# Optimization experiments

Hardware: AMD Instinct MI355X
Metric: run time of the kernel (lower is better)

The kernel has to match this reference:

```python
import jax, jax.numpy as jnp
import numpy as np
import math

B, N, WIDTH, HEADS = 2, 2048, 1024, 16
ATTN_CH = WIDTH // HEADS  # 64 (note: width//heads//3 of the 3*width fused dim)


def setup_inputs() -> dict:
    key = jax.random.key(0)
    ks = jax.random.split(key, 3)
    std = 0.02
    return {
        "x": jax.random.normal(ks[0], (B, N, WIDTH), dtype=jnp.float32),
        "w_qkv": jax.random.normal(ks[1], (WIDTH, 3 * WIDTH), dtype=jnp.float32) * std,
        "b_qkv": jnp.zeros((3 * WIDTH,), dtype=jnp.float32),
        "w_proj": jax.random.normal(ks[2], (WIDTH, WIDTH), dtype=jnp.float32) * std,
        "b_proj": jnp.zeros((WIDTH,), dtype=jnp.float32),
    }


def reference(x, w_qkv, b_qkv, w_proj, b_proj):
    bs, n_ctx, width = x.shape
    qkv = x @ w_qkv + b_qkv                       # [b, n, 3*width]
    attn_ch = (3 * width) // HEADS // 3           # head dim
    scale = 1.0 / math.sqrt(math.sqrt(attn_ch))
    # per-head layout: [b, n, heads, 3*attn_ch] -> split q,k,v
    qkv = qkv.reshape(bs, n_ctx, HEADS, 3 * attn_ch)
    q, k, v = jnp.split(qkv, 3, axis=-1)          # each [b, n, h, c]
    weight = jnp.einsum("bthc,bshc->bhts", q * scale, k * scale)
    weight = jax.nn.softmax(weight.astype(jnp.float32), axis=-1).astype(qkv.dtype)
    out = jnp.einsum("bhts,bshc->bthc", weight, v).reshape(bs, n_ctx, -1)
    return out @ w_proj + b_proj
```

## Files before the change

### kernel.cpp

```cpp
#include <hip/hip_runtime.h>
#include <hip/hip_fp16.h>

#define BATCH 2
#define NCTX  2048
#define WIDTH 1024
#define HEADS 16
#define CH    64
#define QKVD  (3 * WIDTH)
#define MROWS (BATCH * NCTX)

typedef __attribute__((ext_vector_type(4))) float    f32x4;
typedef __attribute__((ext_vector_type(8))) _Float16 f16x8;

#define QSCALE 0.18033688011112042f

__device__ __forceinline__ void gll16(void* lds, const void* g) {
    __builtin_amdgcn_global_load_lds(
        (const __attribute__((address_space(1))) unsigned int*)g,
        (__attribute__((address_space(3))) unsigned int*)lds, 16, 0, 0);
}

__device__ __forceinline__ unsigned pkrtz(float a, float b) {
    auto p = __builtin_amdgcn_cvt_pkrtz(a, b);
    return __builtin_bit_cast(unsigned, p);
}

__global__ __launch_bounds__(256)
void split_x_f16(const float* __restrict__ x, __half* __restrict__ tiles)
{
    const int mb = blockIdx.x, kt = blockIdx.y;
    const int t = threadIdx.x;
    __half* tb = (__half*)tiles + ((size_t)mb * 32 + kt) * 4096;
    #pragma unroll
    for (int it = 0; it < 2; ++it) {
        const int idx = it * 256 + t;
        const int m = idx >> 2, q = idx & 3;
        const float* src = x + (size_t)(mb * 128 + m) * WIDTH + kt * 32 + q * 8;
        const f32x4 v0 = *(const f32x4*)src;
        const f32x4 v1 = *(const f32x4*)(src + 4);
        f16x8 h;
        #pragma unroll
        for (int j = 0; j < 4; ++j) { h[j] = (_Float16)v0[j]; h[4 + j] = (_Float16)v1[j]; }
        *(f16x8*)&tb[(q * 128 + m) * 8] = h;
    }
}

__global__ __launch_bounds__(256)
void split_w_f16(const float* __restrict__ w, __half* __restrict__ tiles, int N)
{
    __shared__ float tile[32][129];
    const int nb = blockIdx.x, kt = blockIdx.y;
    const int t = threadIdx.x;
    #pragma unroll
    for (int it = 0; it < 2; ++it) {
        const int idx = it * 256 + t;
        const int kk = idx >> 4, n8 = idx & 15;
        const float* src = w + (size_t)(kt * 32 + kk) * N + nb * 128 + n8 * 8;
        #pragma unroll
        for (int j = 0; j < 8; ++j) tile[kk][n8 * 8 + j] = src[j];
    }
    __syncthreads();
    __half* tb = tiles + ((size_t)nb * 32 + kt) * 4096;
    #pragma unroll
    for (int it = 0; it < 2; ++it) {
        const int idx = it * 256 + t;
        const int q = idx >> 7, nn = idx & 127;
        f16x8 h;
        #pragma unroll
        for (int j = 0; j < 8; ++j) h[j] = (_Float16)tile[q * 8 + j][nn];
        *(f16x8*)&tb[(q * 128 + nn) * 8] = h;
    }
}

__global__ __launch_bounds__(256)
void gemm_qkv(const __half* __restrict__ At, const __half* __restrict__ Bt,
              const float* __restrict__ bias,
              __half* __restrict__ qg, __half* __restrict__ kg, __half* __restrict__ vtg)
{
    __shared__ __align__(16) _Float16 sm[16384];
    const int t = threadIdx.x, lane = t & 63, w = t >> 6;
    const int lq = lane & 15, quad = lane >> 4;
    const int nb = blockIdx.x, mb = blockIdx.y;
    const int wm = (w >> 1) * 64, wn = (w & 1) * 64;

    const __half* Ab = At + ((size_t)mb * 32) * 4096;
    const __half* Bb = Bt + ((size_t)nb * 32) * 4096;
    const int c0 = w * 4;

    f32x4 acc[4][4];
    #pragma unroll
    for (int i = 0; i < 4; ++i)
        #pragma unroll
        for (int j = 0; j < 4; ++j) acc[i][j] = 0;

    f16x8 pf[4];
    #pragma unroll
    for (int i = 0; i < 4; ++i) {
        const int c = c0 + i;
        const __half* g = (c < 8 ? Ab + c * 512 : Bb + (c - 8) * 512) + lane * 8;
        pf[i] = *(const f16x8*)g;
    }
    #pragma unroll
    for (int i = 0; i < 4; ++i)
        *(f16x8*)&sm[(c0 + i) * 512 + lane * 8] = pf[i];
    __syncthreads();

    for (int kt = 0; kt < 32; ++kt) {
        _Float16* cur = sm + (kt & 1) * 8192;
        _Float16* nxt = sm + ((kt + 1) & 1) * 8192;

        if (kt + 1 < 32) {
            #pragma unroll
            for (int i = 0; i < 4; ++i) {
                const int c = c0 + i;
                const __half* g = (c < 8 ? Ab + (size_t)(kt + 1) * 4096 + c * 512
                                         : Bb + (size_t)(kt + 1) * 4096 + (c - 8) * 512) + lane * 8;
                pf[i] = *(const f16x8*)g;
            }
        }

        f16x8 a[4], b[4];
        #pragma unroll
        for (int i = 0; i < 4; ++i) {
            a[i] = *(const f16x8*)&cur[(quad * 128 + wm + i * 16 + lq) * 8];
            b[i] = *(const f16x8*)&cur[4096 + (quad * 128 + wn + i * 16 + lq) * 8];
        }
        #pragma unroll
        for (int i = 0; i < 4; ++i)
            #pragma unroll
            for (int j = 0; j < 4; ++j)
                acc[i][j] = __builtin_amdgcn_mfma_f32_16x16x32_f16(a[i], b[j], acc[i][j], 0, 0, 0);

        if (kt + 1 < 32) {
            #pragma unroll
            for (int i = 0; i < 4; ++i)
                *(f16x8*)&nxt[(c0 + i) * 512 + lane * 8] = pf[i];
        }
        __syncthreads();
    }

    const int bb = mb >> 4;
    #pragma unroll
    for (int jf = 0; jf < 4; ++jf) {
        const int col = nb * 128 + wn + jf * 16 + lq;
        const int h = col / 192;
        const int sect = col - h * 192;
        const int type = sect >> 6;
        const int c = sect & 63;
        const float bv = bias[col];
        const size_t bh = (size_t)bb * 16 + h;
        #pragma unroll
        for (int i = 0; i < 4; ++i) {
            #pragma unroll
            for (int r = 0; r < 4; ++r) {
                const int n = (mb & 15) * 128 + wm + i * 16 + quad * 4 + r;
                const float v = acc[i][jf][r] + bv;
                if (type == 0) {
                    const size_t a2 = ((bh * 16 + (n >> 7)) * 8 + (c >> 3)) * 1024
                                      + (size_t)(n & 127) * 8 + (c & 7);
                    qg[a2] = __float2half(v * QSCALE);
                } else if (type == 1) {
                    const size_t a2 = ((bh * 32 + (n >> 6)) * 8 + (c >> 3)) * 512
                                      + (size_t)(n & 63) * 8 + (c & 7);
                    kg[a2] = __float2half(v);
                } else {
                    const size_t a2 = ((bh * 32 + (n >> 6)) * 8 + ((n >> 3) & 7)) * 512
                                      + (size_t)c * 8 + (n & 7);
                    vtg[a2] = __float2half(v);
                }
            }
        }
    }
}

__global__ __launch_bounds__(256)
void attn_mfma3(const __half* __restrict__ qg, const __half* __restrict__ kg,
                const __half* __restrict__ vtg, __half* __restrict__ a2)
{
    __shared__ __align__(16) _Float16 Ks[2][4096];
    __shared__ __align__(16) _Float16 Vt[2][4096];
    __shared__ __align__(16) _Float16 Ps[16384];

    const int t = threadIdx.x, lane = t & 63, w = t >> 6;
    const int lq = lane & 15, quad = lane >> 4;
    const int bid = blockIdx.x;
    const int qt2 = (bid >> 3) & 15;
    const int bh_ = (bid & 7) + ((bid >> 7) << 3);
    const size_t bh = (size_t)bh_;
    const int h = bh_ & 15, b = bh_ >> 4;

    const __half* qtile = qg + (bh * 16 + qt2) * 8192;
    const __half* kbase = kg + bh * 32 * 4096;
    const __half* vbase = vtg + bh * 32 * 4096;

    #pragma unroll
    for (int i = 0; i < 4; ++i)
        gll16((void*)&Ps[(w * 4 + i) * 512], (const void*)(qtile + (w * 4 + i) * 512 + lane * 8));

    const int lw = w * 2 * 512 + lane * 8;
    f16x8 kpf[2], vpf[2], vheld[2];
    #pragma unroll
    for (int i = 0; i < 2; ++i) {
        kpf[i] = *(const f16x8*)(kbase + lw + i * 512);
        vpf[i] = *(const f16x8*)(vbase + lw + i * 512);
    }
    __syncthreads();

    #pragma unroll
    for (int i = 0; i < 2; ++i) {
        *(f16x8*)&Ks[0][lw + i * 512] = kpf[i];
        *(f16x8*)&Vt[0][lw + i * 512] = vpf[i];
    }
    f16x8 aq[2][2];
    #pragma unroll
    for (int qn = 0; qn < 2; ++qn)
        #pragma unroll
        for (int ks = 0; ks < 2; ++ks)
            aq[qn][ks] = *(const f16x8*)&Ps[((ks * 4 + quad) * 128 + w * 32 + qn * 16 + lq) * 8];
    __syncthreads();

    f32x4 O[2][4], Ol[2];
    #pragma unroll
    for (int qn = 0; qn < 2; ++qn) {
        Ol[qn] = 0;
        #pragma unroll
        for (int j = 0; j < 4; ++j) O[qn][j] = 0;
    }
    f16x8 ones;
    #pragma unroll
    for (int j = 0; j < 8; ++j) ones[j] = (_Float16)1.0f;

    _Float16* PwBase = &Ps[w * 4096];
    const int kb_hi = quad >> 1, joff = (quad & 1) * 4;
    const f32x4 zc = {0.0f, 0.0f, 0.0f, 0.0f};

    const __half* kp = kbase + 4096 + lw;
    const __half* vp = vbase + 4096 + lw;

    for (int kt = 0; kt < 32; ++kt) {
        const int cur = kt & 1;

        if (kt < 31) {
            kpf[0] = *(const f16x8*)(kp);
            kpf[1] = *(const f16x8*)(kp + 512);
            vpf[0] = *(const f16x8*)(vp);
            vpf[1] = *(const f16x8*)(vp + 512);
            kp += 4096; vp += 4096;
        }

        f32x4 st[4][2];
        #pragma unroll
        for (int mt = 0; mt < 4; ++mt) {
            f16x8 kf0 = *(const f16x8*)&Ks[cur][((quad) * 64 + mt * 16 + lq) * 8];
            f16x8 kf1 = *(const f16x8*)&Ks[cur][((4 + quad) * 64 + mt * 16 + lq) * 8];
            st[mt][0] = __builtin_amdgcn_mfma_f32_16x16x32_f16(kf0, aq[0][0], zc, 0, 0, 0);
            st[mt][1] = __builtin_amdgcn_mfma_f32_16x16x32_f16(kf0, aq[1][0], zc, 0, 0, 0);
            st[mt][0] = __builtin_amdgcn_mfma_f32_16x16x32_f16(kf1, aq[0][1], st[mt][0], 0, 0, 0);
            st[mt][1] = __builtin_amdgcn_mfma_f32_16x16x32_f16(kf1, aq[1][1], st[mt][1], 0, 0, 0);
        }

        if (kt > 0) {
            const int pv = (kt - 1) & 1;
            _Float16* Pr = PwBase + pv * 2048;
            #pragma unroll
            for (int ks = 0; ks < 2; ++ks) {
                f16x8 ap0 = *(const f16x8*)&Pr[((ks * 4 + quad) * 32 + lq) * 8];
                f16x8 ap1 = *(const f16x8*)&Pr[((ks * 4 + quad) * 32 + 16 + lq) * 8];
                Ol[0] = __builtin_amdgcn_mfma_f32_16x16x32_f16(ap0, ones, Ol[0], 0, 0, 0);
                Ol[1] = __builtin_amdgcn_mfma_f32_16x16x32_f16(ap1, ones, Ol[1], 0, 0, 0);
                #pragma unroll
                for (int jc = 0; jc < 4; ++jc) {
                    f16x8 vf = *(const f16x8*)&Vt[pv][((ks * 4 + quad) * 64 + jc * 16 + lq) * 8];
                    O[0][jc] = __builtin_amdgcn_mfma_f32_16x16x32_f16(ap0, vf, O[0][jc], 0, 0, 0);
                    O[1][jc] = __builtin_amdgcn_mfma_f32_16x16x32_f16(ap1, vf, O[1][jc], 0, 0, 0);
                }
            }
        }

        {
            _Float16* Pww = PwBase + cur * 2048;
            #pragma unroll
            for (int mt = 0; mt < 4; ++mt) {
                #pragma unroll
                for (int qn = 0; qn < 2; ++qn) {
                    const float e0 = __builtin_amdgcn_exp2f(st[mt][qn][0]);
                    const float e1 = __builtin_amdgcn_exp2f(st[mt][qn][1]);
                    const float e2 = __builtin_amdgcn_exp2f(st[mt][qn][2]);
                    const float e3 = __builtin_amdgcn_exp2f(st[mt][qn][3]);
                    uint2 pk;
                    pk.x = pkrtz(e0, e1);
                    pk.y = pkrtz(e2, e3);
                    *(uint2*)&Pww[((mt * 2 + kb_hi) * 32 + qn * 16 + lq) * 8 + joff] = pk;
                }
            }
        }

        if (kt < 31) {
            *(f16x8*)&Ks[cur ^ 1][lw] = kpf[0];
            *(f16x8*)&Ks[cur ^ 1][lw + 512] = kpf[1];
        }
        if (kt > 0) {
            *(f16x8*)&Vt[cur][lw] = vheld[0];
            *(f16x8*)&Vt[cur][lw + 512] = vheld[1];
        }
        vheld[0] = vpf[0]; vheld[1] = vpf[1];
        __syncthreads();
    }

    {
        _Float16* Pr = PwBase + 1 * 2048;
        #pragma unroll
        for (int ks = 0; ks < 2; ++ks) {
            f16x8 ap0 = *(const f16x8*)&Pr[((ks * 4 + quad) * 32 + lq) * 8];
            f16x8 ap1 = *(const f16x8*)&Pr[((ks * 4 + quad) * 32 + 16 + lq) * 8];
            Ol[0] = __builtin_amdgcn_mfma_f32_16x16x32_f16(ap0, ones, Ol[0], 0, 0, 0);
            Ol[1] = __builtin_amdgcn_mfma_f32_16x16x32_f16(ap1, ones, Ol[1], 0, 0, 0);
            #pragma unroll
            for (int jc = 0; jc < 4; ++jc) {
                f16x8 vf = *(const f16x8*)&Vt[1][((ks * 4 + quad) * 64 + jc * 16 + lq) * 8];
                O[0][jc] = __builtin_amdgcn_mfma_f32_16x16x32_f16(ap0, vf, O[0][jc], 0, 0, 0);
                O[1][jc] = __builtin_amdgcn_mfma_f32_16x16x32_f16(ap1, vf, O[1][jc], 0, 0, 0);
            }
        }
    }

    float linv[2][4];
    #pragma unroll
    for (int qn = 0; qn < 2; ++qn)
        #pragma unroll
        for (int r = 0; r < 4; ++r)
            linv[qn][r] = 1.0f / Ol[qn][r];

    __half* a2t = a2 + ((size_t)b * 16 + qt2) * 32 * 4096;
    #pragma unroll
    for (int jc = 0; jc < 4; ++jc) {
        const int ch = h * 64 + jc * 16 + lq;
        const int ktp = ch >> 5;
        const int qc = (ch >> 3) & 3;
        const int j = ch & 7;
        #pragma unroll
        for (int qn = 0; qn < 2; ++qn)
            #pragma unroll
            for (int r = 0; r < 4; ++r) {
                const int m = w * 32 + qn * 16 + quad * 4 + r;
                a2t[(size_t)ktp * 4096 + (qc * 128 + m) * 8 + j] =
                    __float2half(O[qn][jc][r] * linv[qn][r]);
            }
    }
}

__global__ __launch_bounds__(256)
void gemm_proj(const __half* __restrict__ At, const __half* __restrict__ Bt,
               const float* __restrict__ bias, float* __restrict__ out)
{
    __shared__ __align__(16) _Float16 sm[16384];
    const int t = threadIdx.x, lane = t & 63, w = t >> 6;
    const int lq = lane & 15, quad = lane >> 4;
    const int nb = blockIdx.x, mb = blockIdx.y;
    const int wm = (w >> 1) * 64, wn = (w & 1) * 64;

    const __half* Ab = At + ((size_t)mb * 32) * 4096;
    const __half* Bb = Bt + ((size_t)nb * 32) * 4096;
    const int c0 = w * 4;

    f32x4 acc[4][4];
    #pragma unroll
    for (int i = 0; i < 4; ++i)
        #pragma unroll
        for (int j = 0; j < 4; ++j) acc[i][j] = 0;

    f16x8 pf[4];
    #pragma unroll
    for (int i = 0; i < 4; ++i) {
        const int c = c0 + i;
        const __half* g = (c < 8 ? Ab + c * 512 : Bb + (c - 8) * 512) + lane * 8;
        pf[i] = *(const f16x8*)g;
    }
    #pragma unroll
    for (int i = 0; i < 4; ++i)
        *(f16x8*)&sm[(c0 + i) * 512 + lane * 8] = pf[i];
    __syncthreads();

    for (int kt = 0; kt < 32; ++kt) {
        _Float16* cur = sm + (kt & 1) * 8192;
        _Float16* nxt = sm + ((kt + 1) & 1) * 8192;

        if (kt + 1 < 32) {
            #pragma unroll
            for (int i = 0; i < 4; ++i) {
                const int c = c0 + i;
                const __half* g = (c < 8 ? Ab + (size_t)(kt + 1) * 4096 + c * 512
                                         : Bb + (size_t)(kt + 1) * 4096 + (c - 8) * 512) + lane * 8;
                pf[i] = *(const f16x8*)g;
            }
        }

        f16x8 a[4], b[4];
        #pragma unroll
        for (int i = 0; i < 4; ++i) {
            a[i] = *(const f16x8*)&cur[(quad * 128 + wm + i * 16 + lq) * 8];
            b[i] = *(const f16x8*)&cur[4096 + (quad * 128 + wn + i * 16 + lq) * 8];
        }
        #pragma unroll
        for (int i = 0; i < 4; ++i)
            #pragma unroll
            for (int j = 0; j < 4; ++j)
                acc[i][j] = __builtin_amdgcn_mfma_f32_16x16x32_f16(a[i], b[j], acc[i][j], 0, 0, 0);

        if (kt + 1 < 32) {
            #pragma unroll
            for (int i = 0; i < 4; ++i)
                *(f16x8*)&nxt[(c0 + i) * 512 + lane * 8] = pf[i];
        }
        __syncthreads();
    }

    #pragma unroll
    for (int jf = 0; jf < 4; ++jf) {
        const int col = nb * 128 + wn + jf * 16 + lq;
        const float bv = bias[col];
        #pragma unroll
        for (int i = 0; i < 4; ++i)
            #pragma unroll
            for (int r = 0; r < 4; ++r) {
                const int row = mb * 128 + wm + i * 16 + quad * 4 + r;
                out[(size_t)row * WIDTH + col] = acc[i][jf][r] + bv;
            }
    }
}

extern "C" void kernel_launch(void* const* d_in, const int* in_sizes, int n_in,
                              void* d_out, int out_size, void* d_ws, size_t ws_size,
                              hipStream_t stream)
{
    const float* x      = (const float*)d_in[0];
    const float* w_qkv  = (const float*)d_in[1];
    const float* b_qkv  = (const float*)d_in[2];
    const float* w_proj = (const float*)d_in[3];
    const float* b_proj = (const float*)d_in[4];
    float* out = (float*)d_out;

    char* p = (char*)d_ws;
    size_t o = 0;
    __half* A1  = (__half*)(p + o); o += (size_t)MROWS * WIDTH * 2;
    __half* Bq  = (__half*)(p + o); o += (size_t)WIDTH * QKVD * 2;
    __half* Qg  = (__half*)(p + o); o += (size_t)MROWS * WIDTH * 2;
    __half* Kg  = (__half*)(p + o); o += (size_t)MROWS * WIDTH * 2;
    __half* Vtg = (__half*)(p + o); o += (size_t)MROWS * WIDTH * 2;
    __half* A2  = (__half*)(p + o); o += (size_t)MROWS * WIDTH * 2;
    __half* Bp  = (__half*)(p + o); o += (size_t)WIDTH * WIDTH * 2;

    dim3 blk(256);

    split_x_f16<<<dim3(32, 32), blk, 0, stream>>>(x, A1);
    split_w_f16<<<dim3(24, 32), blk, 0, stream>>>(w_qkv, Bq, QKVD);
    split_w_f16<<<dim3(8, 32),  blk, 0, stream>>>(w_proj, Bp, WIDTH);

    gemm_qkv<<<dim3(24, 32), blk, 0, stream>>>(A1, Bq, b_qkv, Qg, Kg, Vtg);

    attn_mfma3<<<dim3(512), blk, 0, stream>>>(Qg, Kg, Vtg, A2);

    gemm_proj<<<dim3(8, 32), blk, 0, stream>>>(A2, Bp, b_proj, out);
}
```

Measured before the change: 197.5 us.

## Halve attention query tile per block and drop P double-buffer software pipeline

The attention kernel now processes 64 query rows per block (16 per wave) instead of 128, doubling the grid to 1024 blocks and shrinking the P scratch in LDS from 32KB to 8KB. The cross-iteration pipelining, where the PV product of the previous tile overlapped the QK of the current one, is removed. P is now computed and consumed within the same iteration, and V is stored straight into the next buffer. This aims to raise occupancy and parallelism through lower register and LDS use, at the cost of re-reading K/V twice as often and losing MFMA/exp overlap within a wave.

```diff
diff --git a/kernel.cpp b/kernel.cpp
--- a/kernel.cpp
+++ b/kernel.cpp
@@ -174,31 +174,32 @@
 }
 
 __global__ __launch_bounds__(256)
-void attn_mfma3(const __half* __restrict__ qg, const __half* __restrict__ kg,
+void attn_mfma5(const __half* __restrict__ qg, const __half* __restrict__ kg,
                 const __half* __restrict__ vtg, __half* __restrict__ a2)
 {
     __shared__ __align__(16) _Float16 Ks[2][4096];
     __shared__ __align__(16) _Float16 Vt[2][4096];
-    __shared__ __align__(16) _Float16 Ps[16384];
+    __shared__ __align__(16) _Float16 Ps[4096];
 
     const int t = threadIdx.x, lane = t & 63, w = t >> 6;
     const int lq = lane & 15, quad = lane >> 4;
     const int bid = blockIdx.x;
-    const int qt2 = (bid >> 3) & 15;
-    const int bh_ = (bid & 7) + ((bid >> 7) << 3);
+    const int qt = (bid >> 3) & 31;
+    const int bh_ = (bid & 7) + ((bid >> 8) << 3);
     const size_t bh = (size_t)bh_;
     const int h = bh_ & 15, b = bh_ >> 4;
 
-    const __half* qtile = qg + (bh * 16 + qt2) * 8192;
+    const __half* qtile = qg + (bh * 16 + (qt >> 1)) * 8192 + (size_t)(qt & 1) * 512;
     const __half* kbase = kg + bh * 32 * 4096;
     const __half* vbase = vtg + bh * 32 * 4096;
 
     #pragma unroll
-    for (int i = 0; i < 4; ++i)
-        gll16((void*)&Ps[(w * 4 + i) * 512], (const void*)(qtile + (w * 4 + i) * 512 + lane * 8));
-
-    const int lw = w * 2 * 512 + lane * 8;
-    f16x8 kpf[2], vpf[2], vheld[2];
+    for (int i = 0; i < 2; ++i)
+        gll16((void*)&Ps[(w * 2 + i) * 512],
+              (const void*)(qtile + (size_t)(w * 2 + i) * 1024 + lane * 8));
+
+    const int lw = w * 1024 + lane * 8;
+    f16x8 kpf[2], vpf[2];
     #pragma unroll
     for (int i = 0; i < 2; ++i) {
         kpf[i] = *(const f16x8*)(kbase + lw + i * 512);
@@ -211,26 +212,21 @@
         *(f16x8*)&Ks[0][lw + i * 512] = kpf[i];
         *(f16x8*)&Vt[0][lw + i * 512] = vpf[i];
     }
-    f16x8 aq[2][2];
-    #pragma unroll
-    for (int qn = 0; qn < 2; ++qn)
-        #pragma unroll
-        for (int ks = 0; ks < 2; ++ks)
-            aq[qn][ks] = *(const f16x8*)&Ps[((ks * 4 + quad) * 128 + w * 32 + qn * 16 + lq) * 8];
+    f16x8 aq[2];
+    #pragma unroll
+    for (int ks = 0; ks < 2; ++ks)
+        aq[ks] = *(const f16x8*)&Ps[((ks * 4 + quad) * 64 + w * 16 + lq) * 8];
     __syncthreads();
 
-    f32x4 O[2][4], Ol[2];
-    #pragma unroll
-    for (int qn = 0; qn < 2; ++qn) {
-        Ol[qn] = 0;
-        #pragma unroll
-        for (int j = 0; j < 4; ++j) O[qn][j] = 0;
-    }
+    f32x4 O[4], Ol;
+    Ol = 0;
+    #pragma unroll
+    for (int j = 0; j < 4; ++j) O[j] = 0;
     f16x8 ones;
     #pragma unroll
     for (int j = 0; j < 8; ++j) ones[j] = (_Float16)1.0f;
 
-    _Float16* PwBase = &Ps[w * 4096];
+    _Float16* Pw = &Ps[w * 1024];
     const int kb_hi = quad >> 1, joff = (quad & 1) * 4;
     const f32x4 zc = {0.0f, 0.0f, 0.0f, 0.0f};
 
@@ -248,90 +244,53 @@
             kp += 4096; vp += 4096;
         }
 
-        f32x4 st[4][2];
+        f32x4 st[4];
         #pragma unroll
         for (int mt = 0; mt < 4; ++mt) {
             f16x8 kf0 = *(const f16x8*)&Ks[cur][((quad) * 64 + mt * 16 + lq) * 8];
             f16x8 kf1 = *(const f16x8*)&Ks[cur][((4 + quad) * 64 + mt * 16 + lq) * 8];
-            st[mt][0] = __builtin_amdgcn_mfma_f32_16x16x32_f16(kf0, aq[0][0], zc, 0, 0, 0);
-            st[mt][1] = __builtin_amdgcn_mfma_f32_16x16x32_f16(kf0, aq[1][0], zc, 0, 0, 0);
-            st[mt][0] = __builtin_amdgcn_mfma_f32_16x16x32_f16(kf1, aq[0][1], st[mt][0], 0, 0, 0);
-            st[mt][1] = __builtin_amdgcn_mfma_f32_16x16x32_f16(kf1, aq[1][1], st[mt][1], 0, 0, 0);
-        }
-
-        if (kt > 0) {
-            const int pv = (kt - 1) & 1;
-            _Float16* Pr = PwBase + pv * 2048;
-            #pragma unroll
-            for (int ks = 0; ks < 2; ++ks) {
-                f16x8 ap0 = *(const f16x8*)&Pr[((ks * 4 + quad) * 32 + lq) * 8];
-                f16x8 ap1 = *(const f16x8*)&Pr[((ks * 4 + quad) * 32 + 16 + lq) * 8];
-                Ol[0] = __builtin_amdgcn_mfma_f32_16x16x32_f16(ap0, ones, Ol[0], 0, 0, 0);
-                Ol[1] = __builtin_amdgcn_mfma_f32_16x16x32_f16(ap1, ones, Ol[1], 0, 0, 0);
-                #pragma unroll
-                for (int jc = 0; jc < 4; ++jc) {
-                    f16x8 vf = *(const f16x8*)&Vt[pv][((ks * 4 + quad) * 64 + jc * 16 + lq) * 8];
-                    O[0][jc] = __builtin_amdgcn_mfma_f32_16x16x32_f16(ap0, vf, O[0][jc], 0, 0, 0);
-                    O[1][jc] = __builtin_amdgcn_mfma_f32_16x16x32_f16(ap1, vf, O[1][jc], 0, 0, 0);
-                }
+            st[mt] = __builtin_amdgcn_mfma_f32_16x16x32_f16(kf0, aq[0], zc, 0, 0, 0);
+            st[mt] = __builtin_amdgcn_mfma_f32_16x16x32_f16(kf1, aq[1], st[mt], 0, 0, 0);
+        }
+
+        #pragma unroll
+        for (int mt = 0; mt < 4; ++mt) {
+            const float e0 = __builtin_amdgcn_exp2f(st[mt][0]);
+            const float e1 = __builtin_amdgcn_exp2f(st[mt][1]);
+            const float e2 = __builtin_amdgcn_exp2f(st[mt][2]);
+            const float e3 = __builtin_amdgcn_exp2f(st[mt][3]);
+            uint2 pk;
+            pk.x = pkrtz(e0, e1);
+            pk.y = pkrtz(e2, e3);
+            *(uint2*)&Pw[((mt * 2 + kb_hi) * 16 + lq) * 8 + joff] = pk;
+        }
+
+        #pragma unroll
+        for (int ks = 0; ks < 2; ++ks) {
+            f16x8 ap = *(const f16x8*)&Pw[((ks * 4 + quad) * 16 + lq) * 8];
+            Ol = __builtin_amdgcn_mfma_f32_16x16x32_f16(ap, ones, Ol, 0, 0, 0);
+            #pragma unroll
+            for (int jc = 0; jc < 4; ++jc) {
+                f16x8 vf = *(const f16x8*)&Vt[cur][((ks * 4 + quad) * 64 + jc * 16 + lq) * 8];
+                O[jc] = __builtin_amdgcn_mfma_f32_16x16x32_f16(ap, vf, O[jc], 0, 0, 0);
             }
         }
 
-        {
-            _Float16* Pww = PwBase + cur * 2048;
-            #pragma unroll
-            for (int mt = 0; mt < 4; ++mt) {
-                #pragma unroll
-                for (int qn = 0; qn < 2; ++qn) {
-                    const float e0 = __builtin_amdgcn_exp2f(st[mt][qn][0]);
-                    const float e1 = __builtin_amdgcn_exp2f(st[mt][qn][1]);
-                    const float e2 = __builtin_amdgcn_exp2f(st[mt][qn][2]);
-                    const float e3 = __builtin_amdgcn_exp2f(st[mt][qn][3]);
-                    uint2 pk;
-                    pk.x = pkrtz(e0, e1);
-                    pk.y = pkrtz(e2, e3);
-                    *(uint2*)&Pww[((mt * 2 + kb_hi) * 32 + qn * 16 + lq) * 8 + joff] = pk;
-                }
-            }
-        }
-
         if (kt < 31) {
-            *(f16x8*)&Ks[cur ^ 1][lw] = kpf[0];
+            *(f16x8*)&Ks[cur ^ 1][lw]       = kpf[0];
             *(f16x8*)&Ks[cur ^ 1][lw + 512] = kpf[1];
-        }
-        if (kt > 0) {
-            *(f16x8*)&Vt[cur][lw] = vheld[0];
-            *(f16x8*)&Vt[cur][lw + 512] = vheld[1];
-        }
-        vheld[0] = vpf[0]; vheld[1] = vpf[1];
+            *(f16x8*)&Vt[cur ^ 1][lw]       = vpf[0];
+            *(f16x8*)&Vt[cur ^ 1][lw + 512] = vpf[1];
+        }
         __syncthreads();
     }
 
-    {
-        _Float16* Pr = PwBase + 1 * 2048;
-        #pragma unroll
-        for (int ks = 0; ks < 2; ++ks) {
-            f16x8 ap0 = *(const f16x8*)&Pr[((ks * 4 + quad) * 32 + lq) * 8];
-            f16x8 ap1 = *(const f16x8*)&Pr[((ks * 4 + quad) * 32 + 16 + lq) * 8];
-            Ol[0] = __builtin_amdgcn_mfma_f32_16x16x32_f16(ap0, ones, Ol[0], 0, 0, 0);
-            Ol[1] = __builtin_amdgcn_mfma_f32_16x16x32_f16(ap1, ones, Ol[1], 0, 0, 0);
-            #pragma unroll
-            for (int jc = 0; jc < 4; ++jc) {
-                f16x8 vf = *(const f16x8*)&Vt[1][((ks * 4 + quad) * 64 + jc * 16 + lq) * 8];
-                O[0][jc] = __builtin_amdgcn_mfma_f32_16x16x32_f16(ap0, vf, O[0][jc], 0, 0, 0);
-                O[1][jc] = __builtin_amdgcn_mfma_f32_16x16x32_f16(ap1, vf, O[1][jc], 0, 0, 0);
-            }
-        }
-    }
-
-    float linv[2][4];
-    #pragma unroll
-    for (int qn = 0; qn < 2; ++qn)
-        #pragma unroll
-        for (int r = 0; r < 4; ++r)
-            linv[qn][r] = 1.0f / Ol[qn][r];
-
-    __half* a2t = a2 + ((size_t)b * 16 + qt2) * 32 * 4096;
+    float linv[4];
+    #pragma unroll
+    for (int r = 0; r < 4; ++r) linv[r] = 1.0f / Ol[r];
+
+    __half* a2t = a2 + ((size_t)(b * 16 + (qt >> 1)) * 32) * 4096;
+    const int mbase = (qt & 1) * 64 + w * 16 + quad * 4;
     #pragma unroll
     for (int jc = 0; jc < 4; ++jc) {
         const int ch = h * 64 + jc * 16 + lq;
@@ -339,13 +298,10 @@
         const int qc = (ch >> 3) & 3;
         const int j = ch & 7;
         #pragma unroll
-        for (int qn = 0; qn < 2; ++qn)
-            #pragma unroll
-            for (int r = 0; r < 4; ++r) {
-                const int m = w * 32 + qn * 16 + quad * 4 + r;
-                a2t[(size_t)ktp * 4096 + (qc * 128 + m) * 8 + j] =
-                    __float2half(O[qn][jc][r] * linv[qn][r]);
-            }
+        for (int r = 0; r < 4; ++r) {
+            a2t[(size_t)ktp * 4096 + (qc * 128 + mbase + r) * 8 + j] =
+                __float2half(O[jc][r] * linv[r]);
+        }
     }
 }
 
@@ -458,7 +414,7 @@
 
     gemm_qkv<<<dim3(24, 32), blk, 0, stream>>>(A1, Bq, b_qkv, Qg, Kg, Vtg);
 
-    attn_mfma3<<<dim3(512), blk, 0, stream>>>(Qg, Kg, Vtg, A2);
+    attn_mfma5<<<dim3(1024), blk, 0, stream>>>(Qg, Kg, Vtg, A2);
 
     gemm_proj<<<dim3(8, 32), blk, 0, stream>>>(A2, Bp, b_proj, out);
 }
```

Result: slower. 205.5 us (+4.1%).
